# Kernel optimization log

Hardware: AMD Instinct MI355X
Metric: run time of the kernel (lower is better)

Reference implementation:

```python
import jax, jax.numpy as jnp
import numpy as np

N = 8192
IN_F = 256
OUT_F = 256
ALPHA = 0.2  # LeakyReLU negative slope
NEG_INF = -1e12


def setup_inputs() -> dict:
    key = jax.random.key(0)
    k1, k2, k3, k4, k5 = jax.random.split(key, 5)
    inp = jax.random.normal(k1, (N, IN_F), dtype=jnp.float32)
    adj = jax.random.randint(k2, (N, N), 0, 2, dtype=jnp.int32)
    # xavier_uniform with gain=1.414
    def xavier(k, shape, gain=1.414):
        fan_in, fan_out = shape[0], shape[1]
        bound = gain * np.sqrt(6.0 / (fan_in + fan_out))
        return jax.random.uniform(k, shape, jnp.float32, -bound, bound)
    W = xavier(k3, (IN_F, OUT_F))
    a = xavier(k4, (2 * OUT_F, 1))
    wtrans = xavier(k5, (2 * IN_F, OUT_F))
    return {"inp": inp, "adj": adj, "W": W, "a": a, "wtrans": wtrans}


def reference(inp, adj, W, a, wtrans):
    h = inp @ W                                  # [N, OUT_F]
    Wh1 = h @ a[:OUT_F, :]                       # [N, 1]
    Wh2 = h @ a[OUT_F:, :]                       # [N, 1]
    e = jax.nn.leaky_relu(Wh1 + Wh2.T, ALPHA)    # [N, N]
    mask = adj > 0
    attention = jax.nn.softmax(jnp.where(mask, e, NEG_INF), axis=1)
    negative_attention = -jax.nn.softmax(jnp.where(mask, -e, NEG_INF), axis=1)
    # dropout=0.0 / eval mode -> identity
    h_prime = attention @ inp                    # [N, IN_F]
    h_prime_negative = negative_attention @ inp  # [N, IN_F]
    h_prime_double = jnp.concatenate([h_prime, h_prime_negative], axis=1)
    new_h_prime = h_prime_double @ wtrans        # [N, OUT_F]
    return jax.nn.elu(new_h_prime)               # concat=True
```

## Files before the change

kernel.cpp:

```cpp
#include <hip/hip_runtime.h>
#include <stdint.h>

#define GN 8192
#define LOG2E 1.4426950408889634f

typedef float f32x4 __attribute__((ext_vector_type(4)));
typedef short s16x8 __attribute__((ext_vector_type(8)));
typedef unsigned short u16x8 __attribute__((ext_vector_type(8)));
typedef int i32x4 __attribute__((ext_vector_type(4)));

__device__ __forceinline__ unsigned short f2bf(float f) {
    unsigned int u = __float_as_uint(f);
    u += 0x7FFFu + ((u >> 16) & 1u);
    return (unsigned short)(u >> 16);
}
__device__ __forceinline__ float bf2f(unsigned short h) {
    return __uint_as_float(((unsigned int)h) << 16);
}

__global__ void kA(const float* __restrict__ W, const float* __restrict__ a,
                   float* __restrict__ w1, float* __restrict__ w2) {
    int k = blockIdx.x, l = threadIdx.x;
    float s1 = 0.f, s2 = 0.f;
#pragma unroll
    for (int q = 0; q < 4; ++q) {
        int o = l + q * 64;
        float w = W[k * 256 + o];
        s1 += w * a[o];
        s2 += w * a[256 + o];
    }
#pragma unroll
    for (int off = 32; off; off >>= 1) {
        s1 += __shfl_xor(s1, off);
        s2 += __shfl_xor(s2, off);
    }
    if (l == 0) {
        w1[k] = s1 * LOG2E;
        w2[k] = s2 * LOG2E;
    }
}

__global__ __launch_bounds__(256) void kA2(const float* __restrict__ wt,
                                           unsigned short* __restrict__ wtT) {
    __shared__ unsigned short Tt[32][33];
    const int bi = blockIdx.x;
    const int bj = blockIdx.y;
    const int ty = threadIdx.x >> 3, tx8 = threadIdx.x & 7;
    float4 v = *(const float4*)(wt + (size_t)(bj * 32 + ty) * 256 + bi * 32 + tx8 * 4);
    Tt[tx8 * 4 + 0][ty] = f2bf(v.x);
    Tt[tx8 * 4 + 1][ty] = f2bf(v.y);
    Tt[tx8 * 4 + 2][ty] = f2bf(v.z);
    Tt[tx8 * 4 + 3][ty] = f2bf(v.w);
    __syncthreads();
    ushort4 o4;
    o4.x = Tt[ty][tx8 * 4 + 0];
    o4.y = Tt[ty][tx8 * 4 + 1];
    o4.z = Tt[ty][tx8 * 4 + 2];
    o4.w = Tt[ty][tx8 * 4 + 3];
    *(ushort4*)(wtT + (size_t)(bi * 32 + ty) * 512 + bj * 32 + tx8 * 4) = o4;
}

__global__ __launch_bounds__(256) void kB(const float* __restrict__ inp,
                                          const float* __restrict__ w1,
                                          const float* __restrict__ w2,
                                          float* __restrict__ s, float* __restrict__ t,
                                          unsigned short* __restrict__ inpT) {
    __shared__ unsigned short T[256][33];
    const int tid = threadIdx.x;
    const int r0 = blockIdx.x * 32;
    const int r = tid >> 3, cs = tid & 7;
    const float4* in4 = (const float4*)(inp + (size_t)(r0 + r) * 256 + cs * 32);
    const float4* w14 = (const float4*)(w1 + cs * 32);
    const float4* w24 = (const float4*)(w2 + cs * 32);
    float zs = 0.f, zt = 0.f;
#pragma unroll
    for (int q = 0; q < 8; ++q) {
        float4 v = in4[q];
        float4 a1 = w14[q];
        float4 a2 = w24[q];
        zs += v.x * a1.x + v.y * a1.y + v.z * a1.z + v.w * a1.w;
        zt += v.x * a2.x + v.y * a2.y + v.z * a2.z + v.w * a2.w;
        int c = cs * 32 + q * 4;
        T[c + 0][r] = f2bf(v.x);
        T[c + 1][r] = f2bf(v.y);
        T[c + 2][r] = f2bf(v.z);
        T[c + 3][r] = f2bf(v.w);
    }
#pragma unroll
    for (int off = 1; off < 8; off <<= 1) {
        zs += __shfl_xor(zs, off);
        zt += __shfl_xor(zt, off);
    }
    if (cs == 0) {
        s[r0 + r] = zs;
        t[r0 + r] = zt;
    }
    __syncthreads();
    unsigned short* dst = inpT + (size_t)tid * GN + r0;
    ushort4* d4 = (ushort4*)dst;
#pragma unroll
    for (int q = 0; q < 8; ++q) {
        ushort4 v;
        v.x = T[tid][q * 4 + 0];
        v.y = T[tid][q * 4 + 1];
        v.z = T[tid][q * 4 + 2];
        v.w = T[tid][q * 4 + 3];
        d4[q] = v;
    }
}

#define PROC(AM, TX, BP, BN)                   \
    {                                          \
        float e = sr + (TX);                   \
        float l = fmaxf(e, 0.2f * e);          \
        float p1 = (AM) ? exp2f(l) : 0.f;      \
        float p2 = (AM) ? exp2f(-l) : 0.f;     \
        unsigned short b1 = f2bf(p1);          \
        unsigned short b2 = f2bf(p2);          \
        zp += bf2f(b1);                        \
        zn += bf2f(b2);                        \
        BP = b1;                               \
        BN = b2;                               \
    }

__global__ __launch_bounds__(512, 2) void kC(const int* __restrict__ adj,
                                             const float* __restrict__ sv,
                                             const float* __restrict__ tv,
                                             const unsigned short* __restrict__ inpT,
                                             const unsigned short* __restrict__ wtT,
                                             float* __restrict__ out) {
    __shared__ __align__(16) char smem[16384];
    __shared__ float Zs[32];
    char* ldsP = smem;
    char* ldsN = smem + 8192;
    const int tid = threadIdx.x;
    const int lane = tid & 63, w = tid >> 6;
    const int rr = lane & 15, hi = lane >> 4;
    const int r = tid >> 5, c8 = tid & 31;
    const int i0 = blockIdx.x * 16;
    const float sr = sv[i0 + r];
    float zp = 0.f, zn = 0.f;
    f32x4 accP[2], accN[2];
    accP[0] = (f32x4)(0.f);
    accP[1] = (f32x4)(0.f);
    accN[0] = (f32x4)(0.f);
    accN[1] = (f32x4)(0.f);
    const int fb = w * 32;
    const int wb = (r * 512 + c8 * 16) ^ ((r & 7) << 4);
    const size_t arow = (size_t)(i0 + r) * GN + c8 * 8;
    const float* tb = tv + c8 * 8;

    i32x4 ca0 = __builtin_nontemporal_load((const i32x4*)(adj + arow));
    i32x4 ca1 = __builtin_nontemporal_load((const i32x4*)(adj + arow + 4));
    float4 tf0 = *(const float4*)(tb);
    float4 tf1 = *(const float4*)(tb + 4);

    for (int jc = 0; jc < 32; ++jc) {
        s16x8 bvr[16];
        const unsigned short* bcol = inpT + jc * 256 + hi * 8;
#pragma unroll
        for (int kc = 0; kc < 8; ++kc) {
            bvr[kc * 2 + 0] = *(const s16x8*)(bcol + (size_t)(fb + rr) * GN + kc * 32);
            bvr[kc * 2 + 1] = *(const s16x8*)(bcol + (size_t)(fb + 16 + rr) * GN + kc * 32);
        }
        u16x8 up, un;
        PROC(ca0.x, tf0.x, up[0], un[0]);
        PROC(ca0.y, tf0.y, up[1], un[1]);
        PROC(ca0.z, tf0.z, up[2], un[2]);
        PROC(ca0.w, tf0.w, up[3], un[3]);
        PROC(ca1.x, tf1.x, up[4], un[4]);
        PROC(ca1.y, tf1.y, up[5], un[5]);
        PROC(ca1.z, tf1.z, up[6], un[6]);
        PROC(ca1.w, tf1.w, up[7], un[7]);
        if (jc < 31) {
            const int* an = adj + arow + (jc + 1) * 256;
            ca0 = __builtin_nontemporal_load((const i32x4*)(an));
            ca1 = __builtin_nontemporal_load((const i32x4*)(an + 4));
            const float* tn = tb + (jc + 1) * 256;
            tf0 = *(const float4*)(tn);
            tf1 = *(const float4*)(tn + 4);
        }
        asm volatile("" ::: "memory");
        __builtin_amdgcn_s_barrier();
        asm volatile("" ::: "memory");
        *(u16x8*)(ldsP + wb) = up;
        *(u16x8*)(ldsN + wb) = un;
        asm volatile("s_waitcnt lgkmcnt(0)" ::: "memory");
        __builtin_amdgcn_s_barrier();
        asm volatile("" ::: "memory");
#pragma unroll
        for (int kc = 0; kc < 8; ++kc) {
            int rb = (rr * 512 + kc * 64 + hi * 16) ^ ((rr & 7) << 4);
            s16x8 aP = *(const s16x8*)(ldsP + rb);
            s16x8 aN = *(const s16x8*)(ldsN + rb);
            accP[0] = __builtin_amdgcn_mfma_f32_16x16x32_bf16(aP, bvr[kc * 2 + 0], accP[0], 0, 0, 0);
            accP[1] = __builtin_amdgcn_mfma_f32_16x16x32_bf16(aP, bvr[kc * 2 + 1], accP[1], 0, 0, 0);
            accN[0] = __builtin_amdgcn_mfma_f32_16x16x32_bf16(aN, bvr[kc * 2 + 0], accN[0], 0, 0, 0);
            accN[1] = __builtin_amdgcn_mfma_f32_16x16x32_bf16(aN, bvr[kc * 2 + 1], accN[1], 0, 0, 0);
        }
    }
#pragma unroll
    for (int off = 1; off < 32; off <<= 1) {
        zp += __shfl_xor(zp, off);
        zn += __shfl_xor(zn, off);
    }
    if ((tid & 31) == 0) {
        Zs[r] = zp;
        Zs[16 + r] = zn;
    }
    __syncthreads();
    char* hdl = smem;
#pragma unroll
    for (int reg = 0; reg < 4; ++reg) {
        int row = hi * 4 + reg;
        float izp = 1.f / Zs[row];
        float izn = 1.f / Zs[16 + row];
        int sw = (row & 7) << 4;
#pragma unroll
        for (int nt = 0; nt < 2; ++nt) {
            int col = fb + nt * 16 + rr;
            *(unsigned short*)(hdl + ((row * 1024 + col * 2) ^ sw)) =
                f2bf(accP[nt][reg] * izp);
            *(unsigned short*)(hdl + ((row * 1024 + (col + 256) * 2) ^ sw)) =
                f2bf(-accN[nt][reg] * izn);
        }
    }
    __syncthreads();
    f32x4 oc[2];
    oc[0] = (f32x4)(0.f);
    oc[1] = (f32x4)(0.f);
#pragma unroll
    for (int kc = 0; kc < 16; ++kc) {
        int rb = (rr * 1024 + kc * 64 + hi * 16) ^ ((rr & 7) << 4);
        s16x8 av = *(const s16x8*)(hdl + rb);
#pragma unroll
        for (int nt = 0; nt < 2; ++nt) {
            s16x8 b = *(const s16x8*)(wtT + (size_t)(fb + nt * 16 + rr) * 512 + kc * 32 + hi * 8);
            oc[nt] = __builtin_amdgcn_mfma_f32_16x16x32_bf16(av, b, oc[nt], 0, 0, 0);
        }
    }
#pragma unroll
    for (int nt = 0; nt < 2; ++nt) {
        int col = fb + nt * 16 + rr;
#pragma unroll
        for (int reg = 0; reg < 4; ++reg) {
            int row = i0 + hi * 4 + reg;
            float x = oc[nt][reg];
            out[(size_t)row * 256 + col] = x > 0.f ? x : __expf(x) - 1.f;
        }
    }
}

extern "C" void kernel_launch(void* const* d_in, const int* in_sizes, int n_in,
                              void* d_out, int out_size, void* d_ws, size_t ws_size,
                              hipStream_t stream) {
    const float* inp = (const float*)d_in[0];
    const int* adj = (const int*)d_in[1];
    const float* W = (const float*)d_in[2];
    const float* a = (const float*)d_in[3];
    const float* wt = (const float*)d_in[4];
    float* out = (float*)d_out;
    char* ws = (char*)d_ws;

    unsigned short* inpT = (unsigned short*)ws;
    float* s = (float*)(ws + (4 << 20));
    float* t = (float*)(ws + (4 << 20) + (1 << 15));
    float* w1 = (float*)(ws + (4 << 20) + (2 << 15));
    float* w2 = (float*)(ws + (4 << 20) + (2 << 15) + 4096);
    unsigned short* wtT = (unsigned short*)(ws + (4 << 20) + (2 << 15) + 8192);

    hipLaunchKernelGGL(kA, dim3(256), dim3(64), 0, stream, W, a, w1, w2);
    hipLaunchKernelGGL(kA2, dim3(8, 16), dim3(256), 0, stream, wt, wtT);
    hipLaunchKernelGGL(kB, dim3(256), dim3(256), 0, stream, inp, w1, w2, s, t, inpT);
    hipLaunchKernelGGL(kC, dim3(512), dim3(512), 0, stream, adj, s, t, inpT, wtT, out);
}
```

Baseline: 581.1 us.

## Pack adjacency into LDS bitmasks and double-buffer probability tiles in MFMA-fragment layout

Each thread now converts its 8 adjacency ints into a byte mask stored in LDS, and computes probabilities directly in the MFMA A-fragment layout, so the LDS reads need no swizzle. The probability tiles are double-buffered, which removes one block barrier per iteration. B-operand loads are split into two halves issued around the barrier to overlap global loads with softmax math. Row sums are reduced through a per-wave partial array. In exchange the kernel uses about twice the LDS, which may affect occupancy at 2 blocks per CU.

```diff
diff --git a/kernel.cpp b/kernel.cpp
--- a/kernel.cpp
+++ b/kernel.cpp
@@ -109,18 +109,19 @@
     }
 }
 
-#define PROC(AM, TX, BP, BN)                   \
-    {                                          \
-        float e = sr + (TX);                   \
-        float l = fmaxf(e, 0.2f * e);          \
-        float p1 = (AM) ? exp2f(l) : 0.f;      \
-        float p2 = (AM) ? exp2f(-l) : 0.f;     \
-        unsigned short b1 = f2bf(p1);          \
-        unsigned short b2 = f2bf(p2);          \
-        zp += bf2f(b1);                        \
-        zn += bf2f(b2);                        \
-        BP = b1;                               \
-        BN = b2;                               \
+#define PROCB(Q, TX, BP, BN)                          \
+    {                                                 \
+        float e = sr + (TX);                          \
+        float l = fmaxf(e, 0.2f * e);                 \
+        bool on = (m8 & (1u << (Q))) != 0u;           \
+        float p1 = on ? exp2f(l) : 0.f;               \
+        float p2 = on ? exp2f(-l) : 0.f;              \
+        unsigned short b1 = f2bf(p1);                 \
+        unsigned short b2 = f2bf(p2);                 \
+        zp += bf2f(b1);                               \
+        zn += bf2f(b2);                               \
+        BP = b1;                                      \
+        BN = b2;                                      \
     }
 
 __global__ __launch_bounds__(512, 2) void kC(const int* __restrict__ adj,
@@ -129,16 +130,15 @@
                                              const unsigned short* __restrict__ inpT,
                                              const unsigned short* __restrict__ wtT,
                                              float* __restrict__ out) {
-    __shared__ __align__(16) char smem[16384];
+    __shared__ __align__(16) char smem[33792];
+    __shared__ float Zpart[256];
     __shared__ float Zs[32];
-    char* ldsP = smem;
-    char* ldsN = smem + 8192;
     const int tid = threadIdx.x;
     const int lane = tid & 63, w = tid >> 6;
     const int rr = lane & 15, hi = lane >> 4;
-    const int r = tid >> 5, c8 = tid & 31;
+    const int lr = tid >> 5, lc8 = tid & 31;
     const int i0 = blockIdx.x * 16;
-    const float sr = sv[i0 + r];
+    const float sr = sv[i0 + rr];
     float zp = 0.f, zn = 0.f;
     f32x4 accP[2], accN[2];
     accP[0] = (f32x4)(0.f);
@@ -146,67 +146,107 @@
     accN[0] = (f32x4)(0.f);
     accN[1] = (f32x4)(0.f);
     const int fb = w * 32;
-    const int wb = (r * 512 + c8 * 16) ^ ((r & 7) << 4);
-    const size_t arow = (size_t)(i0 + r) * GN + c8 * 8;
-    const float* tb = tv + c8 * 8;
-
-    i32x4 ca0 = __builtin_nontemporal_load((const i32x4*)(adj + arow));
-    i32x4 ca1 = __builtin_nontemporal_load((const i32x4*)(adj + arow + 4));
-    float4 tf0 = *(const float4*)(tb);
-    float4 tf1 = *(const float4*)(tb + 4);
+    const size_t rowb0 = (size_t)(fb + rr) * GN;
+    const size_t rowb1 = (size_t)(fb + 16 + rr) * GN;
+    const size_t arowb = (size_t)(i0 + lr) * GN + lc8 * 8;
+    const int tspan = w * 32 + hi * 8;
+    const int pwoff = w * 1024 + lane * 16;
+    const int proff = lane * 16;
+    const int moff = 32768;
+    const int mrd = rr * 32 + w * 4 + hi;
+
+    {
+        i32x4 a0 = *(const i32x4*)(adj + arowb);
+        i32x4 a1 = *(const i32x4*)(adj + arowb + 4);
+        unsigned nm = (a0.x ? 1u : 0u) | (a0.y ? 2u : 0u) | (a0.z ? 4u : 0u) | (a0.w ? 8u : 0u) |
+                      (a1.x ? 16u : 0u) | (a1.y ? 32u : 0u) | (a1.z ? 64u : 0u) | (a1.w ? 128u : 0u);
+        *(unsigned char*)(smem + moff + tid) = (unsigned char)nm;
+    }
+    float4 tf0 = *(const float4*)(tv + tspan);
+    float4 tf1 = *(const float4*)(tv + tspan + 4);
+    __syncthreads();
 
     for (int jc = 0; jc < 32; ++jc) {
-        s16x8 bvr[16];
-        const unsigned short* bcol = inpT + jc * 256 + hi * 8;
-#pragma unroll
-        for (int kc = 0; kc < 8; ++kc) {
-            bvr[kc * 2 + 0] = *(const s16x8*)(bcol + (size_t)(fb + rr) * GN + kc * 32);
-            bvr[kc * 2 + 1] = *(const s16x8*)(bcol + (size_t)(fb + 16 + rr) * GN + kc * 32);
-        }
+        const int b8 = (jc & 1) * 8192;
+        const size_t jcoff = (size_t)jc * 256;
+        float4 tc0 = tf0, tc1 = tf1;
+        i32x4 ca0, ca1;
+        if (jc < 31) {
+            const int* an = adj + arowb + (jc + 1) * 256;
+            ca0 = *(const i32x4*)an;
+            ca1 = *(const i32x4*)(an + 4);
+            const float* tn = tv + (jc + 1) * 256 + tspan;
+            tf0 = *(const float4*)tn;
+            tf1 = *(const float4*)(tn + 4);
+        }
+        s16x8 bA[8];
+#pragma unroll
+        for (int kc = 0; kc < 4; ++kc) {
+            bA[kc * 2 + 0] = *(const s16x8*)(inpT + rowb0 + jcoff + kc * 32 + hi * 8);
+            bA[kc * 2 + 1] = *(const s16x8*)(inpT + rowb1 + jcoff + kc * 32 + hi * 8);
+        }
+        __builtin_amdgcn_sched_barrier(0);
+        unsigned m8 = (unsigned)*(volatile unsigned char*)(smem + moff + (jc & 1) * 512 + mrd);
         u16x8 up, un;
-        PROC(ca0.x, tf0.x, up[0], un[0]);
-        PROC(ca0.y, tf0.y, up[1], un[1]);
-        PROC(ca0.z, tf0.z, up[2], un[2]);
-        PROC(ca0.w, tf0.w, up[3], un[3]);
-        PROC(ca1.x, tf1.x, up[4], un[4]);
-        PROC(ca1.y, tf1.y, up[5], un[5]);
-        PROC(ca1.z, tf1.z, up[6], un[6]);
-        PROC(ca1.w, tf1.w, up[7], un[7]);
+        PROCB(0, tc0.x, up[0], un[0]);
+        PROCB(1, tc0.y, up[1], un[1]);
+        PROCB(2, tc0.z, up[2], un[2]);
+        PROCB(3, tc0.w, up[3], un[3]);
+        PROCB(4, tc1.x, up[4], un[4]);
+        PROCB(5, tc1.y, up[5], un[5]);
+        PROCB(6, tc1.z, up[6], un[6]);
+        PROCB(7, tc1.w, up[7], un[7]);
+        *(u16x8*)(smem + b8 + pwoff) = up;
+        *(u16x8*)(smem + 16384 + b8 + pwoff) = un;
         if (jc < 31) {
-            const int* an = adj + arow + (jc + 1) * 256;
-            ca0 = __builtin_nontemporal_load((const i32x4*)(an));
-            ca1 = __builtin_nontemporal_load((const i32x4*)(an + 4));
-            const float* tn = tb + (jc + 1) * 256;
-            tf0 = *(const float4*)(tn);
-            tf1 = *(const float4*)(tn + 4);
-        }
-        asm volatile("" ::: "memory");
-        __builtin_amdgcn_s_barrier();
-        asm volatile("" ::: "memory");
-        *(u16x8*)(ldsP + wb) = up;
-        *(u16x8*)(ldsN + wb) = un;
+            unsigned nm = (ca0.x ? 1u : 0u) | (ca0.y ? 2u : 0u) | (ca0.z ? 4u : 0u) | (ca0.w ? 8u : 0u) |
+                          (ca1.x ? 16u : 0u) | (ca1.y ? 32u : 0u) | (ca1.z ? 64u : 0u) | (ca1.w ? 128u : 0u);
+            *(unsigned char*)(smem + moff + ((jc + 1) & 1) * 512 + tid) = (unsigned char)nm;
+        }
         asm volatile("s_waitcnt lgkmcnt(0)" ::: "memory");
         __builtin_amdgcn_s_barrier();
         asm volatile("" ::: "memory");
-#pragma unroll
-        for (int kc = 0; kc < 8; ++kc) {
-            int rb = (rr * 512 + kc * 64 + hi * 16) ^ ((rr & 7) << 4);
-            s16x8 aP = *(const s16x8*)(ldsP + rb);
-            s16x8 aN = *(const s16x8*)(ldsN + rb);
-            accP[0] = __builtin_amdgcn_mfma_f32_16x16x32_bf16(aP, bvr[kc * 2 + 0], accP[0], 0, 0, 0);
-            accP[1] = __builtin_amdgcn_mfma_f32_16x16x32_bf16(aP, bvr[kc * 2 + 1], accP[1], 0, 0, 0);
-            accN[0] = __builtin_amdgcn_mfma_f32_16x16x32_bf16(aN, bvr[kc * 2 + 0], accN[0], 0, 0, 0);
-            accN[1] = __builtin_amdgcn_mfma_f32_16x16x32_bf16(aN, bvr[kc * 2 + 1], accN[1], 0, 0, 0);
-        }
-    }
-#pragma unroll
-    for (int off = 1; off < 32; off <<= 1) {
-        zp += __shfl_xor(zp, off);
-        zn += __shfl_xor(zn, off);
-    }
-    if ((tid & 31) == 0) {
-        Zs[r] = zp;
-        Zs[16 + r] = zn;
+        s16x8 bB[8];
+#pragma unroll
+        for (int kc = 4; kc < 8; ++kc) {
+            bB[(kc - 4) * 2 + 0] = *(const s16x8*)(inpT + rowb0 + jcoff + kc * 32 + hi * 8);
+            bB[(kc - 4) * 2 + 1] = *(const s16x8*)(inpT + rowb1 + jcoff + kc * 32 + hi * 8);
+        }
+        __builtin_amdgcn_sched_barrier(0);
+#pragma unroll
+        for (int kc = 0; kc < 4; ++kc) {
+            s16x8 aP = *(const s16x8*)(smem + b8 + kc * 1024 + proff);
+            s16x8 aN = *(const s16x8*)(smem + 16384 + b8 + kc * 1024 + proff);
+            accP[0] = __builtin_amdgcn_mfma_f32_16x16x32_bf16(aP, bA[kc * 2 + 0], accP[0], 0, 0, 0);
+            accP[1] = __builtin_amdgcn_mfma_f32_16x16x32_bf16(aP, bA[kc * 2 + 1], accP[1], 0, 0, 0);
+            accN[0] = __builtin_amdgcn_mfma_f32_16x16x32_bf16(aN, bA[kc * 2 + 0], accN[0], 0, 0, 0);
+            accN[1] = __builtin_amdgcn_mfma_f32_16x16x32_bf16(aN, bA[kc * 2 + 1], accN[1], 0, 0, 0);
+        }
+#pragma unroll
+        for (int kc = 4; kc < 8; ++kc) {
+            s16x8 aP = *(const s16x8*)(smem + b8 + kc * 1024 + proff);
+            s16x8 aN = *(const s16x8*)(smem + 16384 + b8 + kc * 1024 + proff);
+            accP[0] = __builtin_amdgcn_mfma_f32_16x16x32_bf16(aP, bB[(kc - 4) * 2 + 0], accP[0], 0, 0, 0);
+            accP[1] = __builtin_amdgcn_mfma_f32_16x16x32_bf16(aP, bB[(kc - 4) * 2 + 1], accP[1], 0, 0, 0);
+            accN[0] = __builtin_amdgcn_mfma_f32_16x16x32_bf16(aN, bB[(kc - 4) * 2 + 0], accN[0], 0, 0, 0);
+            accN[1] = __builtin_amdgcn_mfma_f32_16x16x32_bf16(aN, bB[(kc - 4) * 2 + 1], accN[1], 0, 0, 0);
+        }
+    }
+    zp += __shfl_xor(zp, 16);
+    zp += __shfl_xor(zp, 32);
+    zn += __shfl_xor(zn, 16);
+    zn += __shfl_xor(zn, 32);
+    if (lane < 16) {
+        Zpart[w * 16 + rr] = zp;
+        Zpart[128 + w * 16 + rr] = zn;
+    }
+    __syncthreads();
+    if (tid < 32) {
+        int which = tid >> 4, row = tid & 15;
+        float z = 0.f;
+#pragma unroll
+        for (int w2 = 0; w2 < 8; ++w2) z += Zpart[which * 128 + w2 * 16 + row];
+        Zs[which * 16 + row] = z;
     }
     __syncthreads();
     char* hdl = smem;
```

Measured after the change: 562.0 us. 3.3% less time.
